# Kernel tuning notes

Measured on AMD Instinct MI355X. Metric: run time of the kernel, lower is better.

## Reference

```python
import jax, jax.numpy as jnp
import numpy as np

H = 16          # query heads
KV = 8          # kv heads
D = 256         # head_dim
HID = 3584      # hidden_size
ROPE_BASE = 10000.0
SCALING = 256.0 ** -0.5          # query_pre_attn_scalar ** -0.5
SOFTCAP = 50.0                   # attn_logit_softcapping
WINDOW = 1536 - 1                # sliding_window - 1 (layer_idx 0 is even)


def _rope_neox(x, positions):
    # x: [T, nh, D]; neox style: rotate the two halves of the head dim
    half = D // 2
    inv_freq = 1.0 / (ROPE_BASE ** (jnp.arange(0, D, 2, dtype=jnp.float32) / D))  # [half]
    freqs = positions.astype(jnp.float32)[:, None] * inv_freq[None, :]            # [T, half]
    cos = jnp.cos(freqs)[:, None, :]  # [T, 1, half]
    sin = jnp.sin(freqs)[:, None, :]
    x1, x2 = x[..., :half], x[..., half:]
    return jnp.concatenate([x1 * cos - x2 * sin, x2 * cos + x1 * sin], axis=-1)


def setup_inputs() -> dict:
    key = jax.random.key(0)
    k1, k2, k3 = jax.random.split(key, 3)
    T = 3072
    hidden_states = jax.random.normal(k1, (T, HID), dtype=jnp.float32)
    w_qkv = jax.random.normal(k2, (H * D + 2 * KV * D, HID), dtype=jnp.float32) * 0.02
    w_o = jax.random.normal(k3, (HID, H * D), dtype=jnp.float32) * 0.02
    positions = jnp.arange(T, dtype=jnp.int64)
    return {"positions": positions, "hidden_states": hidden_states,
            "w_qkv": w_qkv, "w_o": w_o}


def reference(positions, hidden_states, w_qkv, w_o):
    T = hidden_states.shape[0]
    qkv = hidden_states @ w_qkv.T                       # [T, (H+2KV)*D]
    q, k, v = jnp.split(qkv, [H * D, H * D + KV * D], axis=-1)
    q = q.reshape(T, H, D)
    k = k.reshape(T, KV, D)
    v = v.reshape(T, KV, D)
    q = _rope_neox(q, positions)
    k = _rope_neox(k, positions)
    # GQA: repeat kv heads (2 query heads per kv head)
    k = jnp.repeat(k, H // KV, axis=1)                  # [T, H, D]
    v = jnp.repeat(v, H // KV, axis=1)
    scores = jnp.einsum('thd,shd->hts', q, k) * SCALING  # [H, T, T]
    scores = SOFTCAP * jnp.tanh(scores / SOFTCAP)       # logit softcapping
    i = positions[:, None]
    j = positions[None, :]
    mask = (j <= i) & (i - j <= WINDOW)                 # causal + sliding window
    scores = jnp.where(mask[None, :, :], scores, -jnp.inf)
    probs = jax.nn.softmax(scores, axis=-1)
    attn = jnp.einsum('hts,shd->thd', probs, v).reshape(T, H * D)
    return attn @ w_o.T                                 # [T, HID]
```

## Files before the change

kernel.cpp:

```cpp
#include <hip/hip_runtime.h>
#include <math.h>

typedef unsigned short u16;
typedef __attribute__((ext_vector_type(8))) short short8;
typedef __attribute__((ext_vector_type(4))) float f32x4;
typedef __attribute__((ext_vector_type(4))) unsigned short u16x4;

#define HN 16
#define KVH 8
#define DH 256
#define HID 3584
#define T_LEN 3072
#define QKV_N 8192
#define O_N 4096
#define WIN 1535
#define SCALING 0.0625f
#define SOFTCAP 50.0f
#define KOFF 4096
#define VOFF 6144
#define PSTR 72
#define NJT 48
#define M_FIX 20.0f

__device__ __forceinline__ u16 f2bf(float f) {
  unsigned u = __float_as_uint(f);
  u += 0x7FFFu + ((u >> 16) & 1u);
  return (u16)(u >> 16);
}
__device__ __forceinline__ float bf2f(u16 b) {
  return __uint_as_float(((unsigned)b) << 16);
}

__device__ __forceinline__ void gload_lds16(const void* g, void* l) {
  __builtin_amdgcn_global_load_lds(
      (const __attribute__((address_space(1))) void*)g,
      (__attribute__((address_space(3))) void*)l, 16, 0, 0);
}

__device__ __forceinline__ f32x4 mfma_bf16(short8 a, short8 b, f32x4 c) {
  return __builtin_amdgcn_mfma_f32_16x16x32_bf16(a, b, c, 0, 0, 0);
}

__global__ __launch_bounds__(256) void cvt_kernel(const float* __restrict__ in,
                                                  u16* __restrict__ out, int n) {
  int i = (blockIdx.x * 256 + threadIdx.x) * 4;
  if (i >= n) return;
  float4 v = *(const float4*)(in + i);
  u16x4 o;
  o[0] = f2bf(v.x); o[1] = f2bf(v.y); o[2] = f2bf(v.z); o[3] = f2bf(v.w);
  *(u16x4*)(out + i) = o;
}

template <int OUT_BF16>
__global__ __launch_bounds__(256) void gemm_bt(const u16* __restrict__ A,
                                               const u16* __restrict__ B,
                                               void* __restrict__ Cv,
                                               int M, int N, int K, int ntn) {
  __shared__ u16 sA[128 * 32];
  __shared__ u16 sB[128 * 32];
  const int bm = blockIdx.x / ntn, bn = blockIdx.x % ntn;
  const int row0 = bm * 128, col0 = bn * 128;
  const int tid = threadIdx.x, lane = tid & 63, w = tid >> 6;
  const int wr = w >> 1, wc = w & 1;
  f32x4 acc[4][4] = {};
  (void)M;

  const u16* Abase = A + (size_t)(row0 + w * 32 + (lane >> 2)) * K + (lane & 3) * 8;
  const u16* Bbase = B + (size_t)(col0 + w * 32 + (lane >> 2)) * K + (lane & 3) * 8;
  u16* sAdst = &sA[w * 32 * 32];
  u16* sBdst = &sB[w * 32 * 32];

  for (int k0 = 0; k0 < K; k0 += 32) {
    gload_lds16(Abase + k0, sAdst);
    gload_lds16(Abase + k0 + (size_t)16 * K, sAdst + 16 * 32);
    gload_lds16(Bbase + k0, sBdst);
    gload_lds16(Bbase + k0 + (size_t)16 * K, sBdst + 16 * 32);
    __syncthreads();

    short8 af[4], bfr[4];
#pragma unroll
    for (int mi = 0; mi < 4; ++mi)
      af[mi] = *(const short8*)&sA[(wr * 64 + mi * 16 + (lane & 15)) * 32 + (lane >> 4) * 8];
#pragma unroll
    for (int ni = 0; ni < 4; ++ni)
      bfr[ni] = *(const short8*)&sB[(wc * 64 + ni * 16 + (lane & 15)) * 32 + (lane >> 4) * 8];
#pragma unroll
    for (int mi = 0; mi < 4; ++mi)
#pragma unroll
      for (int ni = 0; ni < 4; ++ni)
        acc[mi][ni] = mfma_bf16(af[mi], bfr[ni], acc[mi][ni]);
    __syncthreads();
  }

#pragma unroll
  for (int mi = 0; mi < 4; ++mi) {
#pragma unroll
    for (int ni = 0; ni < 4; ++ni) {
      const int r = row0 + wr * 64 + mi * 16 + (lane >> 4) * 4;
      const int c = col0 + wc * 64 + ni * 16 + (lane & 15);
#pragma unroll
      for (int j = 0; j < 4; ++j) {
        float v = acc[mi][ni][j];
        if (OUT_BF16)
          ((u16*)Cv)[(size_t)(r + j) * N + c] = f2bf(v);
        else
          ((float*)Cv)[(size_t)(r + j) * N + c] = v;
      }
    }
  }
}

__global__ __launch_bounds__(256) void rope_kernel(u16* __restrict__ qkv) {
  int idx = blockIdx.x * 256 + threadIdx.x;
  int d = idx & 127;
  int hh = (idx >> 7) % 24;
  int t = idx / (24 * 128);
  if (t >= T_LEN) return;
  size_t base = (size_t)t * QKV_N + (hh < HN ? hh * DH : HN * DH + (hh - HN) * DH);
  float inv = exp2f((float)d * (-13.287712379549449f / 128.0f));
  float ang = (float)t * inv;
  float s = sinf(ang), c = cosf(ang);
  float x1 = bf2f(qkv[base + d]);
  float x2 = bf2f(qkv[base + d + 128]);
  qkv[base + d] = f2bf(x1 * c - x2 * s);
  qkv[base + d + 128] = f2bf(x2 * c + x1 * s);
}

__global__ __launch_bounds__(256) void vtrans_kernel(const u16* __restrict__ qkv,
                                                     u16* __restrict__ vt) {
  __shared__ u16 tile[256 * 72];
  const int jb = blockIdx.x * 64;
  const int kvh = blockIdx.y;
  const int tid = threadIdx.x;
  const int t = tid & 63, dc = tid >> 6;

  const u16* src = qkv + (size_t)(jb + t) * QKV_N + VOFF + kvh * DH + dc * 64;
#pragma unroll
  for (int i = 0; i < 8; ++i) {
    short8 v = *(const short8*)(src + i * 8);
    int d0 = dc * 64 + i * 8;
#pragma unroll
    for (int j = 0; j < 8; ++j) tile[(d0 + j) * 72 + t] = (u16)(short)v[j];
  }
  __syncthreads();

  u16* dst = vt + ((size_t)kvh * NJT + blockIdx.x) * 16384;
#pragma unroll
  for (int s = 0; s < 8; ++s) {
    int G = s * 256 + tid;
    int d = G >> 3, g = G & 7;
    short8 x = *(const short8*)&tile[d * 72 + ((g ^ (d & 7)) * 8)];
    *(short8*)(dst + G * 8) = x;
  }
}

__global__ __launch_bounds__(256) void attn_kernel(const u16* __restrict__ qkv,
                                                   const u16* __restrict__ vt,
                                                   u16* __restrict__ po,
                                                   float* __restrict__ ml) {
  const int wg = blockIdx.x;
  const int kvh = wg & 7;
  const int rest = wg >> 3;
  const int qt = rest >> 2;
  const int c = (rest >> 1) & 1;
  const int h = kvh * 2 + (rest & 1);
  const int qb = qt * 64;
  const int tid = threadIdx.x, lane = tid & 63, w = tid >> 6;

  __shared__ u16 sK[64 * 256];
  __shared__ u16 sVt[64 * 256];
  __shared__ u16 sP[4][16 * PSTR];

  int jmin = qb - WIN; if (jmin < 0) jmin = 0;
  const int jt0 = jmin >> 6, jt1 = qb >> 6;
  const int nt = jt1 - jt0 + 1;
  const int half = (nt + 1) >> 1;
  const int t_beg = (c == 0) ? jt0 : jt0 + half;
  const int t_end = (c == 0) ? jt0 + half : jt1 + 1;

  const int qrow = qb + w * 16 + (lane & 15);
  short8 qf[8];
  {
    const u16* qp = qkv + (size_t)qrow * QKV_N + h * DH + (lane >> 4) * 8;
#pragma unroll
    for (int kc = 0; kc < 8; ++kc) qf[kc] = *(const short8*)(qp + kc * 32);
  }

  f32x4 O[16];
#pragma unroll
  for (int i = 0; i < 16; ++i) O[i] = f32x4{0.f, 0.f, 0.f, 0.f};
  float lrow[4] = {0.f, 0.f, 0.f, 0.f};

  const int dl = lane & 15;
  const int vb0 = dl * 64 + (((lane >> 4)) ^ (dl & 7)) * 8;
  const int vb1 = dl * 64 + (((lane >> 4) + 4) ^ (dl & 7)) * 8;

  for (int jt = t_beg; jt < t_end; ++jt) {
    const int jb = jt * 64;
#pragma unroll
    for (int i = 0; i < 8; ++i) {
      int rl = w * 16 + i * 2 + (lane >> 5);
      int g = (lane & 31) ^ (rl & 7);
      gload_lds16(qkv + (size_t)(jb + rl) * QKV_N + KOFF + kvh * DH + g * 8,
                  &sK[(w * 16 + i * 2) * 256]);
    }
    {
      const u16* vtile = vt + ((size_t)kvh * NJT + jt) * 16384;
#pragma unroll
      for (int s = 0; s < 8; ++s) {
        int id = w * 8 + s;
        gload_lds16(vtile + id * 512 + lane * 8, &sVt[id * 512]);
      }
    }
    __syncthreads();

    f32x4 S[4];
#pragma unroll
    for (int nf = 0; nf < 4; ++nf) S[nf] = f32x4{0.f, 0.f, 0.f, 0.f};
#pragma unroll
    for (int nf = 0; nf < 4; ++nf) {
      int krow = nf * 16 + (lane & 15);
#pragma unroll
      for (int kc = 0; kc < 8; ++kc) {
        int g = (kc * 4 + (lane >> 4)) ^ (krow & 7);
        short8 kf = *(const short8*)&sK[krow * 256 + g * 8];
        S[nf] = mfma_bf16(qf[kc], kf, S[nf]);
      }
    }

#pragma unroll
    for (int r = 0; r < 4; ++r) {
      const int irow = qb + w * 16 + (lane >> 4) * 4 + r;
      const int ql = (lane >> 4) * 4 + r;
#pragma unroll
      for (int nf = 0; nf < 4; ++nf) {
        int j = jb + nf * 16 + (lane & 15);
        float x = S[nf][r] * (SCALING / SOFTCAP);
        float e2 = __expf(-2.0f * fabsf(x));
        float th = (1.0f - e2) / (1.0f + e2);
        th = x >= 0.0f ? th : -th;
        float val = SOFTCAP * th;
        bool ok = (j <= irow) && (irow - j <= WIN);
        float p = ok ? __expf(val - M_FIX) : 0.0f;
        lrow[r] += p;
        sP[w][ql * PSTR + nf * 16 + (lane & 15)] = f2bf(p);
      }
    }

    short8 pf0 = *(const short8*)&sP[w][(lane & 15) * PSTR + (lane >> 4) * 8];
    short8 pf1 = *(const short8*)&sP[w][(lane & 15) * PSTR + 32 + (lane >> 4) * 8];
#pragma unroll
    for (int nf = 0; nf < 16; ++nf) {
      short8 vf0 = *(const short8*)&sVt[nf * 1024 + vb0];
      short8 vf1 = *(const short8*)&sVt[nf * 1024 + vb1];
      O[nf] = mfma_bf16(pf0, vf0, O[nf]);
      O[nf] = mfma_bf16(pf1, vf1, O[nf]);
    }
    __syncthreads();
  }

#pragma unroll
  for (int r = 0; r < 4; ++r) {
#pragma unroll
    for (int off = 8; off >= 1; off >>= 1) lrow[r] += __shfl_xor(lrow[r], off);
  }

#pragma unroll
  for (int nf = 0; nf < 16; ++nf) {
    int d = nf * 16 + (lane & 15);
#pragma unroll
    for (int r = 0; r < 4; ++r) {
      int trow = qb + w * 16 + (lane >> 4) * 4 + r;
      po[(((size_t)c * T_LEN + trow) * HN + h) * DH + d] = f2bf(O[nf][r]);
    }
  }
  if ((lane & 15) == 0) {
#pragma unroll
    for (int r = 0; r < 4; ++r) {
      int trow = qb + w * 16 + (lane >> 4) * 4 + r;
      size_t mi = (((size_t)c * T_LEN + trow) * HN + h) * 2;
      ml[mi] = M_FIX;
      ml[mi + 1] = lrow[r];
    }
  }
}

__global__ __launch_bounds__(256) void combine_kernel(const u16* __restrict__ po,
                                                      const float* __restrict__ ml,
                                                      u16* __restrict__ attnb) {
  const int t = blockIdx.x;
  const int h = threadIdx.x >> 4;
  const int d0 = (threadIdx.x & 15) * 16;
  const size_t row = (size_t)t * HN + h;
  const float l0 = ml[row * 2 + 1];
  const float l1 = ml[(size_t)T_LEN * HN * 2 + row * 2 + 1];
  const float inv = 1.0f / (l0 + l1);
  const size_t i0 = row * DH + d0;
  const size_t i1 = (size_t)T_LEN * HN * DH + i0;
#pragma unroll
  for (int half = 0; half < 2; ++half) {
    short8 x0 = *(const short8*)(po + i0 + half * 8);
    short8 x1 = *(const short8*)(po + i1 + half * 8);
    short8 o;
#pragma unroll
    for (int j = 0; j < 8; ++j)
      o[j] = (short)f2bf((bf2f((u16)x0[j]) + bf2f((u16)x1[j])) * inv);
    *(short8*)(attnb + i0 + half * 8) = o;
  }
}

extern "C" void kernel_launch(void* const* d_in, const int* in_sizes, int n_in,
                              void* d_out, int out_size, void* d_ws, size_t ws_size,
                              hipStream_t stream) {
  const float* hidden = (const float*)d_in[1];
  const float* w_qkv = (const float*)d_in[2];
  const float* w_o = (const float*)d_in[3];
  float* out = (float*)d_out;
  char* ws = (char*)d_ws;

  u16* wqkvb = (u16*)(ws);
  u16* po = (u16*)(ws);
  float* ml = (float*)(ws + 50331648);
  u16* attnb = (u16*)(ws);
  u16* hb = (u16*)(ws + 58720256);
  u16* vtb = (u16*)(ws + 58720256);
  u16* qkvb = (u16*)(ws + 80740352);
  u16* wob = (u16*)(ws + 80740352);

  {
    int n = T_LEN * HID;
    cvt_kernel<<<dim3((n / 4 + 255) / 256), 256, 0, stream>>>(hidden, hb, n);
  }
  {
    int n = QKV_N * HID;
    cvt_kernel<<<dim3((n / 4 + 255) / 256), 256, 0, stream>>>(w_qkv, wqkvb, n);
  }
  gemm_bt<1><<<dim3(24 * 64), 256, 0, stream>>>(hb, wqkvb, qkvb, T_LEN, QKV_N, HID, 64);
  {
    int n = T_LEN * 24 * 128;
    rope_kernel<<<dim3(n / 256), 256, 0, stream>>>(qkvb);
  }
  vtrans_kernel<<<dim3(NJT, KVH), 256, 0, stream>>>(qkvb, vtb);
  attn_kernel<<<dim3(1536), 256, 0, stream>>>(qkvb, vtb, po, ml);
  {
    int n = HID * O_N;
    cvt_kernel<<<dim3((n / 4 + 255) / 256), 256, 0, stream>>>(w_o, wob, n);
  }
  combine_kernel<<<dim3(T_LEN), 256, 0, stream>>>(po, ml, attnb);
  gemm_bt<0><<<dim3(24 * 28), 256, 0, stream>>>(attnb, wob, out, T_LEN, HID, O_N, 28);
}
```

Measured before the change: 630.3 us.

## Replace GEMM with 256x256 double-buffered, swizzled 8-wave bf16 MFMA kernel

Rewrites both projection GEMMs to use 256x256 tiles with 8 waves, a K-step of 64, and double-buffered LDS fed by direct global-to-LDS loads. An XOR swizzle avoids LDS bank conflicts, and an explicit vmcnt wait lets the next tile's loads overlap with the current tile's MFMAs. Block IDs are remapped across 8 XCD groups so neighbouring tiles share L2. The larger tiles raise operand reuse, but they use 128 KB of LDS and more registers, and give fewer blocks (384 and 168), so some CUs may sit idle.

```diff
diff --git a/kernel.cpp b/kernel.cpp
--- a/kernel.cpp
+++ b/kernel.cpp
@@ -52,51 +52,90 @@
 }
 
 template <int OUT_BF16>
-__global__ __launch_bounds__(256) void gemm_bt(const u16* __restrict__ A,
-                                               const u16* __restrict__ B,
-                                               void* __restrict__ Cv,
-                                               int M, int N, int K, int ntn) {
-  __shared__ u16 sA[128 * 32];
-  __shared__ u16 sB[128 * 32];
-  const int bm = blockIdx.x / ntn, bn = blockIdx.x % ntn;
-  const int row0 = bm * 128, col0 = bn * 128;
-  const int tid = threadIdx.x, lane = tid & 63, w = tid >> 6;
-  const int wr = w >> 1, wc = w & 1;
-  f32x4 acc[4][4] = {};
-  (void)M;
-
-  const u16* Abase = A + (size_t)(row0 + w * 32 + (lane >> 2)) * K + (lane & 3) * 8;
-  const u16* Bbase = B + (size_t)(col0 + w * 32 + (lane >> 2)) * K + (lane & 3) * 8;
-  u16* sAdst = &sA[w * 32 * 32];
-  u16* sBdst = &sB[w * 32 * 32];
-
-  for (int k0 = 0; k0 < K; k0 += 32) {
-    gload_lds16(Abase + k0, sAdst);
-    gload_lds16(Abase + k0 + (size_t)16 * K, sAdst + 16 * 32);
-    gload_lds16(Bbase + k0, sBdst);
-    gload_lds16(Bbase + k0 + (size_t)16 * K, sBdst + 16 * 32);
-    __syncthreads();
-
-    short8 af[4], bfr[4];
-#pragma unroll
-    for (int mi = 0; mi < 4; ++mi)
-      af[mi] = *(const short8*)&sA[(wr * 64 + mi * 16 + (lane & 15)) * 32 + (lane >> 4) * 8];
-#pragma unroll
-    for (int ni = 0; ni < 4; ++ni)
-      bfr[ni] = *(const short8*)&sB[(wc * 64 + ni * 16 + (lane & 15)) * 32 + (lane >> 4) * 8];
-#pragma unroll
-    for (int mi = 0; mi < 4; ++mi)
-#pragma unroll
-      for (int ni = 0; ni < 4; ++ni)
-        acc[mi][ni] = mfma_bf16(af[mi], bfr[ni], acc[mi][ni]);
-    __syncthreads();
-  }
-
-#pragma unroll
-  for (int mi = 0; mi < 4; ++mi) {
+__global__ __launch_bounds__(512, 2) void gemm8(const u16* __restrict__ A,
+                                                const u16* __restrict__ B,
+                                                void* __restrict__ Cv,
+                                                int N, int K, int ntn, int cpx) {
+  __shared__ u16 sA[2][256 * 64];
+  __shared__ u16 sB[2][256 * 64];
+
+  const int bid = blockIdx.x;
+  const int wg = (bid & 7) * cpx + (bid >> 3);
+  const int bm = wg / ntn, bn = wg % ntn;
+  const int row0 = bm * 256, col0 = bn * 256;
+  const int tid = threadIdx.x, lane = tid & 63, wid = tid >> 6;
+  const int wr = wid >> 2, wc = wid & 3;
+
+  const int srow = lane >> 3;
+  const int sg = (lane & 7) ^ srow;
+  const u16* Asrc = A + (size_t)(row0 + wid * 32 + srow) * K + sg * 8;
+  const u16* Bsrc = B + (size_t)(col0 + wid * 32 + srow) * K + sg * 8;
+  const size_t rK8 = (size_t)8 * K;
+
+  f32x4 acc[8][4] = {};
+  const int NT = K >> 6;
+
+#pragma unroll
+  for (int i = 0; i < 4; ++i) {
+    gload_lds16(Asrc + i * rK8, &sA[0][(wid * 4 + i) * 512]);
+    gload_lds16(Bsrc + i * rK8, &sB[0][(wid * 4 + i) * 512]);
+  }
+
+  const int fr = lane & 15;
+  const int g0 = (lane >> 4) ^ (lane & 7);
+  const int g1 = (4 + (lane >> 4)) ^ (lane & 7);
+
+  for (int t = 0; t < NT; ++t) {
+    const int d = t & 1;
+    if (t + 1 < NT) {
+      const u16* As = Asrc + (size_t)(t + 1) * 64;
+      const u16* Bs = Bsrc + (size_t)(t + 1) * 64;
+#pragma unroll
+      for (int i = 0; i < 4; ++i) {
+        gload_lds16(As + i * rK8, &sA[d ^ 1][(wid * 4 + i) * 512]);
+        gload_lds16(Bs + i * rK8, &sB[d ^ 1][(wid * 4 + i) * 512]);
+      }
+      __builtin_amdgcn_sched_barrier(0);
+      asm volatile("s_waitcnt vmcnt(8)" ::: "memory");
+    } else {
+      asm volatile("s_waitcnt vmcnt(0)" ::: "memory");
+    }
+    __builtin_amdgcn_sched_barrier(0);
+    __builtin_amdgcn_s_barrier();
+    __builtin_amdgcn_sched_barrier(0);
+
+    __builtin_amdgcn_s_setprio(1);
+#pragma unroll
+    for (int kk = 0; kk < 2; ++kk) {
+      const int gk = kk ? g1 : g0;
+      short8 af[8];
+#pragma unroll
+      for (int mi = 0; mi < 8; ++mi)
+        af[mi] = *(const short8*)&sA[d][(wr * 128 + mi * 16 + fr) * 64 + gk * 8];
+#pragma unroll
+      for (int nh = 0; nh < 2; ++nh) {
+        short8 bf[2];
+#pragma unroll
+        for (int nb = 0; nb < 2; ++nb)
+          bf[nb] = *(const short8*)&sB[d][(wc * 64 + (nh * 2 + nb) * 16 + fr) * 64 + gk * 8];
+#pragma unroll
+        for (int mi = 0; mi < 8; ++mi)
+#pragma unroll
+          for (int nb = 0; nb < 2; ++nb)
+            acc[mi][nh * 2 + nb] = mfma_bf16(af[mi], bf[nb], acc[mi][nh * 2 + nb]);
+      }
+    }
+    __builtin_amdgcn_s_setprio(0);
+    __builtin_amdgcn_sched_barrier(0);
+    __builtin_amdgcn_s_barrier();
+    __builtin_amdgcn_sched_barrier(0);
+  }
+
+#pragma unroll
+  for (int mi = 0; mi < 8; ++mi) {
 #pragma unroll
     for (int ni = 0; ni < 4; ++ni) {
-      const int r = row0 + wr * 64 + mi * 16 + (lane >> 4) * 4;
+      const int r = row0 + wr * 128 + mi * 16 + (lane >> 4) * 4;
       const int c = col0 + wc * 64 + ni * 16 + (lane & 15);
 #pragma unroll
       for (int j = 0; j < 4; ++j) {
@@ -335,7 +374,7 @@
     int n = QKV_N * HID;
     cvt_kernel<<<dim3((n / 4 + 255) / 256), 256, 0, stream>>>(w_qkv, wqkvb, n);
   }
-  gemm_bt<1><<<dim3(24 * 64), 256, 0, stream>>>(hb, wqkvb, qkvb, T_LEN, QKV_N, HID, 64);
+  gemm8<1><<<dim3(384), 512, 0, stream>>>(hb, wqkvb, qkvb, QKV_N, HID, 32, 48);
   {
     int n = T_LEN * 24 * 128;
     rope_kernel<<<dim3(n / 256), 256, 0, stream>>>(qkvb);
@@ -347,5 +386,5 @@
     cvt_kernel<<<dim3((n / 4 + 255) / 256), 256, 0, stream>>>(w_o, wob, n);
   }
   combine_kernel<<<dim3(T_LEN), 256, 0, stream>>>(po, ml, attnb);
-  gemm_bt<0><<<dim3(24 * 28), 256, 0, stream>>>(attnb, wob, out, T_LEN, HID, O_N, 28);
-}
+  gemm8<0><<<dim3(168), 512, 0, stream>>>(attnb, wob, out, HID, O_N, 14, 21);
+}
```

Measured after the change: 583.2 us. -7.5%, faster.
